# Performance work log

Measured on AMD Instinct MI355X. Metric: run time of the kernel, lower is better.

## Reference

```python
import jax, jax.numpy as jnp
import numpy as np

B, S = 4096, 256
D = 32  # output_size // 4


def setup_inputs() -> dict:
    key = jax.random.key(0)
    ks = jax.random.split(key, 32)
    # continuous features
    cont_p = jax.random.normal(ks[0], (B, S, 3), dtype=jnp.float32)
    cont_c = jax.random.normal(ks[1], (B, S, 2), dtype=jnp.float32)
    # categorical features, per-column vocab sizes from Embedding tables
    vocabs_p = [2, 2, 2, 11, 34]
    cat_p = jnp.stack([
        jax.random.randint(ks[2 + i], (B, S), 0, v, dtype=jnp.int32)
        for i, v in enumerate(vocabs_p)], axis=2)
    vocabs_c = [19, 31]
    cat_c = jnp.stack([
        jax.random.randint(ks[7 + i], (B, S), 0, v, dtype=jnp.int32)
        for i, v in enumerate(vocabs_c)], axis=2)
    lengths = jax.random.randint(ks[9], (B,), 1, S + 1, dtype=jnp.int32)

    def lin(k, fan_in, fan_out):
        bound = 1.0 / np.sqrt(fan_in)
        kw, kb = jax.random.split(k)
        w = jax.random.uniform(kw, (fan_in, fan_out), jnp.float32, -bound, bound)
        b = jax.random.uniform(kb, (fan_out,), jnp.float32, -bound, bound)
        return w, b

    w_p1, b_p1 = lin(ks[10], 3, D)
    w_p2, b_p2 = lin(ks[11], D, D)
    w_c1, b_c1 = lin(ks[12], 2, D)
    w_c2, b_c2 = lin(ks[13], D, D)
    emb_gender = jax.random.normal(ks[14], (2, D), dtype=jnp.float32)
    emb_korean = jax.random.normal(ks[15], (2, D), dtype=jnp.float32)
    emb_primary = jax.random.normal(ks[16], (2, D), dtype=jnp.float32)
    emb_job = jax.random.normal(ks[17], (11, D), dtype=jnp.float32)
    emb_rep = jax.random.normal(ks[18], (34, D), dtype=jnp.float32)
    emb_place = jax.random.normal(ks[19], (19, D), dtype=jnp.float32)
    emb_add = jax.random.normal(ks[20], (31, D), dtype=jnp.float32)
    w_fc1, b_fc1 = lin(ks[21], 128, 64)
    w_fc2, b_fc2 = lin(ks[22], 64, 2)

    return dict(cont_p=cont_p, cont_c=cont_c, cat_p=cat_p, cat_c=cat_c,
                lengths=lengths,
                w_p1=w_p1, b_p1=b_p1, w_p2=w_p2, b_p2=b_p2,
                w_c1=w_c1, b_c1=b_c1, w_c2=w_c2, b_c2=b_c2,
                emb_gender=emb_gender, emb_korean=emb_korean,
                emb_primary=emb_primary, emb_job=emb_job, emb_rep=emb_rep,
                emb_place=emb_place, emb_add=emb_add,
                w_fc1=w_fc1, b_fc1=b_fc1, w_fc2=w_fc2, b_fc2=b_fc2)


def reference(cont_p, cont_c, cat_p, cat_c, lengths,
              w_p1, b_p1, w_p2, b_p2, w_c1, b_c1, w_c2, b_c2,
              emb_gender, emb_korean, emb_primary, emb_job, emb_rep,
              emb_place, emb_add, w_fc1, b_fc1, w_fc2, b_fc2):
    # small per-token MLPs on continuous features -> [B,S,D]
    hp = jax.nn.relu(cont_p @ w_p1 + b_p1) @ w_p2 + b_p2
    hc = jax.nn.relu(cont_c @ w_c1 + b_c1) @ w_c2 + b_c2
    # multi-table embedding lookups, averaged per group -> [B,S,D]
    ep = (emb_gender[cat_p[:, :, 0]] + emb_korean[cat_p[:, :, 1]] +
          emb_primary[cat_p[:, :, 2]] + emb_job[cat_p[:, :, 3]] +
          emb_rep[cat_p[:, :, 4]]) / 5.0
    ec = (emb_place[cat_c[:, :, 0]] + emb_add[cat_c[:, :, 1]]) / 2.0
    # concat order matches torch: (cat_p, cat_c, cont_p, cont_c) -> [B,S,128]
    x = jnp.concatenate([ep, ec, hp, hc], axis=2)
    # ragged mean pool over first lengths[i] positions (masked segment mean)
    mask = (jnp.arange(x.shape[1])[None, :] < lengths[:, None])
    pooled = jnp.sum(x * mask[:, :, None], axis=1) / lengths[:, None].astype(x.dtype)
    # head: relu(fc1) -> relu(fc2); dropout p=0.0 is identity
    h = jax.nn.relu(pooled @ w_fc1 + b_fc1)
    return jax.nn.relu(h @ w_fc2 + b_fc2)
```

## Files before the change

kernel.cpp:

```cpp
#include <hip/hip_runtime.h>


#define BDIM 256

__global__ __launch_bounds__(BDIM, 8)
void mlpreg_kernel(const float* __restrict__ cont_p,
                   const float* __restrict__ cont_c,
                   const int* __restrict__ cat_p,
                   const int* __restrict__ cat_c,
                   const int* __restrict__ lengths,
                   const float* __restrict__ w_p1, const float* __restrict__ b_p1,
                   const float* __restrict__ w_p2, const float* __restrict__ b_p2,
                   const float* __restrict__ w_c1, const float* __restrict__ b_c1,
                   const float* __restrict__ w_c2, const float* __restrict__ b_c2,
                   const float* __restrict__ emb_g,  const float* __restrict__ emb_k,
                   const float* __restrict__ emb_pr, const float* __restrict__ emb_j,
                   const float* __restrict__ emb_r,  const float* __restrict__ emb_pl,
                   const float* __restrict__ emb_a,
                   const float* __restrict__ w_fc1, const float* __restrict__ b_fc1,
                   const float* __restrict__ w_fc2, const float* __restrict__ b_fc2,
                   float* __restrict__ out)
{
    constexpr int S = 256;
    __shared__ float sContP[S * 3];
    __shared__ float sContC[S * 2];
    __shared__ int   hist[96];
    __shared__ int   sBin[4][3];
    __shared__ float sRedP[128], sRedC[128];
    __shared__ float sPacc[64];
    __shared__ float sPooled[128];
    __shared__ float sRedF[BDIM];

    const int tid = threadIdx.x;
    const int b   = blockIdx.x;
    int L = lengths[b];
    if (L < 1) L = 1;
    if (L > S) L = S;
    const float invL = 1.0f / (float)L;
    const float Lf   = (float)L;

    const int*   kp = cat_p  + (size_t)b * (S * 5);
    const int*   kc = cat_c  + (size_t)b * (S * 2);
    const float* gp = cont_p + (size_t)b * (S * 3);
    const float* gc = cont_c + (size_t)b * (S * 2);

    const int n3 = 3 * L, n2 = 2 * L, n5 = 5 * L;
    float rp0 = (tid       < n3) ? gp[tid]       : 0.f;
    float rp1 = (tid + 256 < n3) ? gp[tid + 256] : 0.f;
    float rp2 = (tid + 512 < n3) ? gp[tid + 512] : 0.f;
    float rc0 = (tid       < n2) ? gc[tid]       : 0.f;
    float rc1 = (tid + 256 < n2) ? gc[tid + 256] : 0.f;
    int rk[5];
    #pragma unroll
    for (int j = 0; j < 5; ++j) {
        int ii = tid + 256 * j;
        rk[j] = (ii < n5) ? kp[ii] : -1;
    }
    int rq0 = (tid       < n2) ? kc[tid]       : -1;
    int rq1 = (tid + 256 < n2) ? kc[tid + 256] : -1;

    if (tid < 96) hist[tid] = 0;
    __syncthreads();

    if (tid       < n3) sContP[tid]       = rp0;
    if (tid + 256 < n3) sContP[tid + 256] = rp1;
    if (tid + 512 < n3) sContP[tid + 512] = rp2;
    if (tid       < n2) sContC[tid]       = rc0;
    if (tid + 256 < n2) sContC[tid + 256] = rc1;

    int sg = 0, sk = 0, spr = 0;
    #pragma unroll
    for (int j = 0; j < 5; ++j) {
        int ii = tid + 256 * j;
        if (ii < n5) {
            int col = ii % 5, v = rk[j];
            if      (col == 0) sg  += v;
            else if (col == 1) sk  += v;
            else if (col == 2) spr += v;
            else if (col == 3) atomicAdd(&hist[v], 1);
            else               atomicAdd(&hist[11 + v], 1);
        }
    }
    if (rq0 >= 0) atomicAdd(&hist[((tid & 1) ? 64 : 45) + rq0], 1);
    if (rq1 >= 0) atomicAdd(&hist[((tid & 1) ? 64 : 45) + rq1], 1);

    #pragma unroll
    for (int d = 32; d; d >>= 1) {
        sg  += __shfl_xor(sg,  d);
        sk  += __shfl_xor(sk,  d);
        spr += __shfl_xor(spr, d);
    }
    const int wv = tid >> 6, lane = tid & 63;
    if (lane == 0) { sBin[wv][0] = sg; sBin[wv][1] = sk; sBin[wv][2] = spr; }
    __syncthreads();

    const int g8 = tid >> 5, ch = tid & 31, h = lane >> 5;
    const float wp0 = w_p1[ch], wp1 = w_p1[32 + ch], wp2 = w_p1[64 + ch], bp = b_p1[ch];
    const float wc0 = w_c1[ch], wc1 = w_c1[32 + ch], bc = b_c1[ch];
    float accP = 0.f, accC = 0.f;
    #pragma unroll 2
    for (int t = g8; t < L; t += 8) {
        float c0 = sContP[3 * t], c1 = sContP[3 * t + 1], c2 = sContP[3 * t + 2];
        float d0 = sContC[2 * t], d1 = sContC[2 * t + 1];
        accP += fmaxf(fmaf(c0, wp0, fmaf(c1, wp1, fmaf(c2, wp2, bp))), 0.f);
        accC += fmaxf(fmaf(d0, wc0, fmaf(d1, wc1, bc)), 0.f);
    }
    accP += __shfl_down(accP, 32);
    accC += __shfl_down(accC, 32);
    if (lane < 32) { sRedP[wv * 32 + ch] = accP; sRedC[wv * 32 + ch] = accC; }
    __syncthreads();

    if (wv == 0) {
        float sgT  = (float)(sBin[0][0] + sBin[1][0] + sBin[2][0] + sBin[3][0]);
        float skT  = (float)(sBin[0][1] + sBin[1][1] + sBin[2][1] + sBin[3][1]);
        float sprT = (float)(sBin[0][2] + sBin[1][2] + sBin[2][2] + sBin[3][2]);
        float s = 0.f;
        if (h == 0) {
            s  = fmaf(Lf - sgT,  emb_g[ch],  sgT  * emb_g[32 + ch]);
            s += fmaf(Lf - sprT, emb_pr[ch], sprT * emb_pr[32 + ch]);
            #pragma unroll
            for (int r = 0; r < 6; ++r)  s = fmaf((float)hist[r],      emb_j[r * 32 + ch], s);
            #pragma unroll
            for (int r = 0; r < 17; ++r) s = fmaf((float)hist[11 + r], emb_r[r * 32 + ch], s);
        } else {
            s = fmaf(Lf - skT, emb_k[ch], skT * emb_k[32 + ch]);
            #pragma unroll
            for (int r = 6; r < 11; ++r)  s = fmaf((float)hist[r],      emb_j[r * 32 + ch], s);
            #pragma unroll
            for (int r = 17; r < 34; ++r) s = fmaf((float)hist[11 + r], emb_r[r * 32 + ch], s);
        }
        s += __shfl_down(s, 32);
        if (h == 0) sPooled[ch] = s * (invL * 0.2f);
    } else if (wv == 1) {
        float s = 0.f;
        if (h == 0) {
            #pragma unroll
            for (int r = 0; r < 10; ++r) s = fmaf((float)hist[45 + r], emb_pl[r * 32 + ch], s);
            #pragma unroll
            for (int r = 0; r < 16; ++r) s = fmaf((float)hist[64 + r], emb_a[r * 32 + ch], s);
        } else {
            #pragma unroll
            for (int r = 10; r < 19; ++r) s = fmaf((float)hist[45 + r], emb_pl[r * 32 + ch], s);
            #pragma unroll
            for (int r = 16; r < 31; ++r) s = fmaf((float)hist[64 + r], emb_a[r * 32 + ch], s);
        }
        s += __shfl_down(s, 32);
        if (h == 0) sPooled[32 + ch] = s * (invL * 0.5f);
    } else if (wv == 2) {
        if (lane < 32)
            sPacc[ch] = (sRedP[ch] + sRedP[32 + ch] + sRedP[64 + ch] + sRedP[96 + ch]) * invL;
    } else {
        if (lane < 32)
            sPacc[32 + ch] = (sRedC[ch] + sRedC[32 + ch] + sRedC[64 + ch] + sRedC[96 + ch]) * invL;
    }
    __syncthreads();

    if (wv == 2) {
        const int kb = h * 16;
        float v = (h == 0) ? b_p2[ch] : 0.f;
        #pragma unroll
        for (int k = 0; k < 16; ++k) v = fmaf(sPacc[kb + k], w_p2[(kb + k) * 32 + ch], v);
        v += __shfl_down(v, 32);
        if (h == 0) sPooled[64 + ch] = v;
    } else if (wv == 3) {
        const int kb = h * 16;
        float v = (h == 0) ? b_c2[ch] : 0.f;
        #pragma unroll
        for (int k = 0; k < 16; ++k) v = fmaf(sPacc[32 + kb + k], w_c2[(kb + k) * 32 + ch], v);
        v += __shfl_down(v, 32);
        if (h == 0) sPooled[96 + ch] = v;
    }
    __syncthreads();

    {
        const int o = tid & 63, part = tid >> 6;
        const float* wk = w_fc1 + (size_t)(part * 32) * 64 + o;
        const float* xk = sPooled + part * 32;
        float v0 = 0.f, v1 = 0.f, v2 = 0.f, v3 = 0.f;
        #pragma unroll
        for (int k = 0; k < 32; k += 4) {
            v0 = fmaf(xk[k + 0], wk[(size_t)(k + 0) * 64], v0);
            v1 = fmaf(xk[k + 1], wk[(size_t)(k + 1) * 64], v1);
            v2 = fmaf(xk[k + 2], wk[(size_t)(k + 2) * 64], v2);
            v3 = fmaf(xk[k + 3], wk[(size_t)(k + 3) * 64], v3);
        }
        sRedF[tid] = (v0 + v1) + (v2 + v3);
    }
    __syncthreads();

    if (wv == 0) {
        float hv = b_fc1[lane] + (sRedF[lane] + sRedF[64 + lane])
                               + (sRedF[128 + lane] + sRedF[192 + lane]);
        hv = fmaxf(hv, 0.f);
        float p0 = hv * w_fc2[lane * 2 + 0];
        float p1 = hv * w_fc2[lane * 2 + 1];
        #pragma unroll
        for (int d = 32; d; d >>= 1) {
            p0 += __shfl_xor(p0, d);
            p1 += __shfl_xor(p1, d);
        }
        if (lane == 0) {
            float2 o2;
            o2.x = fmaxf(p0 + b_fc2[0], 0.f);
            o2.y = fmaxf(p1 + b_fc2[1], 0.f);
            *(float2*)&out[(size_t)b * 2] = o2;
        }
    }
}

extern "C" void kernel_launch(void* const* d_in, const int* in_sizes, int n_in,
                              void* d_out, int out_size, void* d_ws, size_t ws_size,
                              hipStream_t stream) {
    const float* cont_p = (const float*)d_in[0];
    const float* cont_c = (const float*)d_in[1];
    const int*   cat_p  = (const int*)d_in[2];
    const int*   cat_c  = (const int*)d_in[3];
    const int*   lens   = (const int*)d_in[4];
    const float* w_p1   = (const float*)d_in[5];
    const float* b_p1   = (const float*)d_in[6];
    const float* w_p2   = (const float*)d_in[7];
    const float* b_p2   = (const float*)d_in[8];
    const float* w_c1   = (const float*)d_in[9];
    const float* b_c1   = (const float*)d_in[10];
    const float* w_c2   = (const float*)d_in[11];
    const float* b_c2   = (const float*)d_in[12];
    const float* emb_g  = (const float*)d_in[13];
    const float* emb_k  = (const float*)d_in[14];
    const float* emb_pr = (const float*)d_in[15];
    const float* emb_j  = (const float*)d_in[16];
    const float* emb_r  = (const float*)d_in[17];
    const float* emb_pl = (const float*)d_in[18];
    const float* emb_a  = (const float*)d_in[19];
    const float* w_fc1  = (const float*)d_in[20];
    const float* b_fc1  = (const float*)d_in[21];
    const float* w_fc2  = (const float*)d_in[22];
    const float* b_fc2  = (const float*)d_in[23];
    float* out = (float*)d_out;

    const int B = 4096;
    hipLaunchKernelGGL(mlpreg_kernel, dim3(B), dim3(BDIM), 0, stream,
                       cont_p, cont_c, cat_p, cat_c, lens,
                       w_p1, b_p1, w_p2, b_p2, w_c1, b_c1, w_c2, b_c2,
                       emb_g, emb_k, emb_pr, emb_j, emb_r, emb_pl, emb_a,
                       w_fc1, b_fc1, w_fc2, b_fc2, out);
}
```

Before: 148.8 us.

## Process four rows per block with register prefetch and split histograms

Each block now handles four batch rows in sequence. While the current row is being computed, the next row's inputs are loaded into registers, so global-load latency overlaps with compute. The shared histogram is duplicated per wave pair to reduce atomic contention, and the final fc1 layer is batched across the four rows so each weight load is reused four times. In exchange the grid shrinks to a quarter of the blocks and the min-blocks launch bound is dropped, which lowers the number of resident waves available to hide latency.

New measurement: 152.6 us. 2.6% more time.

```diff
diff --git a/kernel.cpp b/kernel.cpp
--- a/kernel.cpp
+++ b/kernel.cpp
@@ -2,8 +2,34 @@
 
 
 #define BDIM 256
-
-__global__ __launch_bounds__(BDIM, 8)
+#define RPB 4
+
+struct RowRegs {
+    float p0, p1, p2, c0, c1;
+    int   k0, k1, k2, k3, k4, q0, q1;
+};
+
+__device__ __forceinline__ RowRegs load_row(const float* gp, const float* gc,
+                                            const int* kp, const int* kc,
+                                            int tid, int L) {
+    RowRegs r;
+    const int n3 = 3 * L, n2 = 2 * L, n5 = 5 * L;
+    r.p0 = (tid       < n3) ? gp[tid]       : 0.f;
+    r.p1 = (tid + 256 < n3) ? gp[tid + 256] : 0.f;
+    r.p2 = (tid + 512 < n3) ? gp[tid + 512] : 0.f;
+    r.c0 = (tid       < n2) ? gc[tid]       : 0.f;
+    r.c1 = (tid + 256 < n2) ? gc[tid + 256] : 0.f;
+    r.k0 = (tid        < n5) ? kp[tid]        : -1;
+    r.k1 = (tid + 256  < n5) ? kp[tid + 256]  : -1;
+    r.k2 = (tid + 512  < n5) ? kp[tid + 512]  : -1;
+    r.k3 = (tid + 768  < n5) ? kp[tid + 768]  : -1;
+    r.k4 = (tid + 1024 < n5) ? kp[tid + 1024] : -1;
+    r.q0 = (tid       < n2) ? kc[tid]       : -1;
+    r.q1 = (tid + 256 < n2) ? kc[tid + 256] : -1;
+    return r;
+}
+
+__global__ __launch_bounds__(BDIM)
 void mlpreg_kernel(const float* __restrict__ cont_p,
                    const float* __restrict__ cont_c,
                    const int* __restrict__ cat_p,
@@ -24,186 +50,187 @@
     constexpr int S = 256;
     __shared__ float sContP[S * 3];
     __shared__ float sContC[S * 2];
-    __shared__ int   hist[96];
+    __shared__ int   hist[2][96];
     __shared__ int   sBin[4][3];
     __shared__ float sRedP[128], sRedC[128];
     __shared__ float sPacc[64];
-    __shared__ float sPooled[128];
-    __shared__ float sRedF[BDIM];
-
-    const int tid = threadIdx.x;
-    const int b   = blockIdx.x;
-    int L = lengths[b];
-    if (L < 1) L = 1;
-    if (L > S) L = S;
-    const float invL = 1.0f / (float)L;
-    const float Lf   = (float)L;
-
-    const int*   kp = cat_p  + (size_t)b * (S * 5);
-    const int*   kc = cat_c  + (size_t)b * (S * 2);
-    const float* gp = cont_p + (size_t)b * (S * 3);
-    const float* gc = cont_c + (size_t)b * (S * 2);
-
-    const int n3 = 3 * L, n2 = 2 * L, n5 = 5 * L;
-    float rp0 = (tid       < n3) ? gp[tid]       : 0.f;
-    float rp1 = (tid + 256 < n3) ? gp[tid + 256] : 0.f;
-    float rp2 = (tid + 512 < n3) ? gp[tid + 512] : 0.f;
-    float rc0 = (tid       < n2) ? gc[tid]       : 0.f;
-    float rc1 = (tid + 256 < n2) ? gc[tid + 256] : 0.f;
-    int rk[5];
+    __shared__ float sPooled[RPB][128];
+    __shared__ float sF[4][RPB][64];
+
+    const int tid  = threadIdx.x;
+    const int wv   = tid >> 6, lane = tid & 63;
+    const int ch   = tid & 31, h = lane >> 5, g8 = tid >> 5;
+    const int base = blockIdx.x * RPB;
+
+    int Ls[RPB];
     #pragma unroll
-    for (int j = 0; j < 5; ++j) {
-        int ii = tid + 256 * j;
-        rk[j] = (ii < n5) ? kp[ii] : -1;
-    }
-    int rq0 = (tid       < n2) ? kc[tid]       : -1;
-    int rq1 = (tid + 256 < n2) ? kc[tid + 256] : -1;
-
-    if (tid < 96) hist[tid] = 0;
-    __syncthreads();
-
-    if (tid       < n3) sContP[tid]       = rp0;
-    if (tid + 256 < n3) sContP[tid + 256] = rp1;
-    if (tid + 512 < n3) sContP[tid + 512] = rp2;
-    if (tid       < n2) sContC[tid]       = rc0;
-    if (tid + 256 < n2) sContC[tid + 256] = rc1;
-
-    int sg = 0, sk = 0, spr = 0;
+    for (int r = 0; r < RPB; ++r) {
+        int L = lengths[base + r];
+        Ls[r] = (L < 1) ? 1 : (L > S ? S : L);
+    }
+    const float* gpA[RPB]; const float* gcA[RPB];
+    const int*   kpA[RPB]; const int*   kcA[RPB];
     #pragma unroll
-    for (int j = 0; j < 5; ++j) {
-        int ii = tid + 256 * j;
-        if (ii < n5) {
-            int col = ii % 5, v = rk[j];
-            if      (col == 0) sg  += v;
-            else if (col == 1) sk  += v;
-            else if (col == 2) spr += v;
-            else if (col == 3) atomicAdd(&hist[v], 1);
-            else               atomicAdd(&hist[11 + v], 1);
-        }
-    }
-    if (rq0 >= 0) atomicAdd(&hist[((tid & 1) ? 64 : 45) + rq0], 1);
-    if (rq1 >= 0) atomicAdd(&hist[((tid & 1) ? 64 : 45) + rq1], 1);
-
-    #pragma unroll
-    for (int d = 32; d; d >>= 1) {
-        sg  += __shfl_xor(sg,  d);
-        sk  += __shfl_xor(sk,  d);
-        spr += __shfl_xor(spr, d);
-    }
-    const int wv = tid >> 6, lane = tid & 63;
-    if (lane == 0) { sBin[wv][0] = sg; sBin[wv][1] = sk; sBin[wv][2] = spr; }
-    __syncthreads();
-
-    const int g8 = tid >> 5, ch = tid & 31, h = lane >> 5;
+    for (int r = 0; r < RPB; ++r) {
+        gpA[r] = cont_p + (size_t)(base + r) * (S * 3);
+        gcA[r] = cont_c + (size_t)(base + r) * (S * 2);
+        kpA[r] = cat_p  + (size_t)(base + r) * (S * 5);
+        kcA[r] = cat_c  + (size_t)(base + r) * (S * 2);
+    }
     const float wp0 = w_p1[ch], wp1 = w_p1[32 + ch], wp2 = w_p1[64 + ch], bp = b_p1[ch];
     const float wc0 = w_c1[ch], wc1 = w_c1[32 + ch], bc = b_c1[ch];
-    float accP = 0.f, accC = 0.f;
-    #pragma unroll 2
-    for (int t = g8; t < L; t += 8) {
-        float c0 = sContP[3 * t], c1 = sContP[3 * t + 1], c2 = sContP[3 * t + 2];
-        float d0 = sContC[2 * t], d1 = sContC[2 * t + 1];
-        accP += fmaxf(fmaf(c0, wp0, fmaf(c1, wp1, fmaf(c2, wp2, bp))), 0.f);
-        accC += fmaxf(fmaf(d0, wc0, fmaf(d1, wc1, bc)), 0.f);
-    }
-    accP += __shfl_down(accP, 32);
-    accC += __shfl_down(accC, 32);
-    if (lane < 32) { sRedP[wv * 32 + ch] = accP; sRedC[wv * 32 + ch] = accC; }
+
+    for (int i = tid; i < 192; i += BDIM) ((int*)hist)[i] = 0;
+
+    RowRegs cur = load_row(gpA[0], gcA[0], kpA[0], kcA[0], tid, Ls[0]);
     __syncthreads();
 
-    if (wv == 0) {
-        float sgT  = (float)(sBin[0][0] + sBin[1][0] + sBin[2][0] + sBin[3][0]);
-        float skT  = (float)(sBin[0][1] + sBin[1][1] + sBin[2][1] + sBin[3][1]);
-        float sprT = (float)(sBin[0][2] + sBin[1][2] + sBin[2][2] + sBin[3][2]);
-        float s = 0.f;
-        if (h == 0) {
-            s  = fmaf(Lf - sgT,  emb_g[ch],  sgT  * emb_g[32 + ch]);
-            s += fmaf(Lf - sprT, emb_pr[ch], sprT * emb_pr[32 + ch]);
-            #pragma unroll
-            for (int r = 0; r < 6; ++r)  s = fmaf((float)hist[r],      emb_j[r * 32 + ch], s);
-            #pragma unroll
-            for (int r = 0; r < 17; ++r) s = fmaf((float)hist[11 + r], emb_r[r * 32 + ch], s);
-        } else {
-            s = fmaf(Lf - skT, emb_k[ch], skT * emb_k[32 + ch]);
-            #pragma unroll
-            for (int r = 6; r < 11; ++r)  s = fmaf((float)hist[r],      emb_j[r * 32 + ch], s);
-            #pragma unroll
-            for (int r = 17; r < 34; ++r) s = fmaf((float)hist[11 + r], emb_r[r * 32 + ch], s);
-        }
-        s += __shfl_down(s, 32);
-        if (h == 0) sPooled[ch] = s * (invL * 0.2f);
-    } else if (wv == 1) {
-        float s = 0.f;
-        if (h == 0) {
-            #pragma unroll
-            for (int r = 0; r < 10; ++r) s = fmaf((float)hist[45 + r], emb_pl[r * 32 + ch], s);
-            #pragma unroll
-            for (int r = 0; r < 16; ++r) s = fmaf((float)hist[64 + r], emb_a[r * 32 + ch], s);
-        } else {
-            #pragma unroll
-            for (int r = 10; r < 19; ++r) s = fmaf((float)hist[45 + r], emb_pl[r * 32 + ch], s);
-            #pragma unroll
-            for (int r = 16; r < 31; ++r) s = fmaf((float)hist[64 + r], emb_a[r * 32 + ch], s);
-        }
-        s += __shfl_down(s, 32);
-        if (h == 0) sPooled[32 + ch] = s * (invL * 0.5f);
-    } else if (wv == 2) {
-        if (lane < 32)
-            sPacc[ch] = (sRedP[ch] + sRedP[32 + ch] + sRedP[64 + ch] + sRedP[96 + ch]) * invL;
-    } else {
-        if (lane < 32)
-            sPacc[32 + ch] = (sRedC[ch] + sRedC[32 + ch] + sRedC[64 + ch] + sRedC[96 + ch]) * invL;
-    }
-    __syncthreads();
-
-    if (wv == 2) {
-        const int kb = h * 16;
-        float v = (h == 0) ? b_p2[ch] : 0.f;
-        #pragma unroll
-        for (int k = 0; k < 16; ++k) v = fmaf(sPacc[kb + k], w_p2[(kb + k) * 32 + ch], v);
-        v += __shfl_down(v, 32);
-        if (h == 0) sPooled[64 + ch] = v;
-    } else if (wv == 3) {
-        const int kb = h * 16;
-        float v = (h == 0) ? b_c2[ch] : 0.f;
-        #pragma unroll
-        for (int k = 0; k < 16; ++k) v = fmaf(sPacc[32 + kb + k], w_c2[(kb + k) * 32 + ch], v);
-        v += __shfl_down(v, 32);
-        if (h == 0) sPooled[96 + ch] = v;
-    }
-    __syncthreads();
-
-    {
-        const int o = tid & 63, part = tid >> 6;
-        const float* wk = w_fc1 + (size_t)(part * 32) * 64 + o;
-        const float* xk = sPooled + part * 32;
-        float v0 = 0.f, v1 = 0.f, v2 = 0.f, v3 = 0.f;
-        #pragma unroll
-        for (int k = 0; k < 32; k += 4) {
-            v0 = fmaf(xk[k + 0], wk[(size_t)(k + 0) * 64], v0);
-            v1 = fmaf(xk[k + 1], wk[(size_t)(k + 1) * 64], v1);
-            v2 = fmaf(xk[k + 2], wk[(size_t)(k + 2) * 64], v2);
-            v3 = fmaf(xk[k + 3], wk[(size_t)(k + 3) * 64], v3);
-        }
-        sRedF[tid] = (v0 + v1) + (v2 + v3);
-    }
-    __syncthreads();
-
-    if (wv == 0) {
-        float hv = b_fc1[lane] + (sRedF[lane] + sRedF[64 + lane])
-                               + (sRedF[128 + lane] + sRedF[192 + lane]);
-        hv = fmaxf(hv, 0.f);
-        float p0 = hv * w_fc2[lane * 2 + 0];
-        float p1 = hv * w_fc2[lane * 2 + 1];
+    #pragma unroll
+    for (int r = 0; r < RPB; ++r) {
+        const int   L    = Ls[r];
+        const float Lf   = (float)L;
+        const float invL = 1.0f / Lf;
+
+        sContP[tid]       = cur.p0;
+        sContP[tid + 256] = cur.p1;
+        sContP[tid + 512] = cur.p2;
+        sContC[tid]       = cur.c0;
+        sContC[tid + 256] = cur.c1;
+
+        int sg = 0, sk = 0, spr = 0;
+        int* hc = hist[wv >> 1];
+        {
+            int c0 = tid % 5;
+            int c1 = (c0 + 1) % 5, c2 = (c0 + 2) % 5, c3 = (c0 + 3) % 5, c4 = (c0 + 4) % 5;
+            int v;
+            v = cur.k0; if (v >= 0) { if (c0 == 0) sg += v; else if (c0 == 1) sk += v; else if (c0 == 2) spr += v; else if (c0 == 3) atomicAdd(&hc[v], 1); else atomicAdd(&hc[11 + v], 1); }
+            v = cur.k1; if (v >= 0) { if (c1 == 0) sg += v; else if (c1 == 1) sk += v; else if (c1 == 2) spr += v; else if (c1 == 3) atomicAdd(&hc[v], 1); else atomicAdd(&hc[11 + v], 1); }
+            v = cur.k2; if (v >= 0) { if (c2 == 0) sg += v; else if (c2 == 1) sk += v; else if (c2 == 2) spr += v; else if (c2 == 3) atomicAdd(&hc[v], 1); else atomicAdd(&hc[11 + v], 1); }
+            v = cur.k3; if (v >= 0) { if (c3 == 0) sg += v; else if (c3 == 1) sk += v; else if (c3 == 2) spr += v; else if (c3 == 3) atomicAdd(&hc[v], 1); else atomicAdd(&hc[11 + v], 1); }
+            v = cur.k4; if (v >= 0) { if (c4 == 0) sg += v; else if (c4 == 1) sk += v; else if (c4 == 2) spr += v; else if (c4 == 3) atomicAdd(&hc[v], 1); else atomicAdd(&hc[11 + v], 1); }
+        }
+        if (cur.q0 >= 0) atomicAdd(&hc[((tid & 1) ? 64 : 45) + cur.q0], 1);
+        if (cur.q1 >= 0) atomicAdd(&hc[((tid & 1) ? 64 : 45) + cur.q1], 1);
         #pragma unroll
         for (int d = 32; d; d >>= 1) {
-            p0 += __shfl_xor(p0, d);
-            p1 += __shfl_xor(p1, d);
-        }
+            sg += __shfl_xor(sg, d); sk += __shfl_xor(sk, d); spr += __shfl_xor(spr, d);
+        }
+        if (lane == 0) { sBin[wv][0] = sg; sBin[wv][1] = sk; sBin[wv][2] = spr; }
+        __syncthreads();
+
+        RowRegs nxt;
+        if (r + 1 < RPB)
+            nxt = load_row(gpA[r + 1], gcA[r + 1], kpA[r + 1], kcA[r + 1], tid, Ls[r + 1]);
+
+        float accP = 0.f, accC = 0.f;
+        #pragma unroll 2
+        for (int t = g8; t < L; t += 8) {
+            float c0 = sContP[3 * t], c1 = sContP[3 * t + 1], c2 = sContP[3 * t + 2];
+            float d0 = sContC[2 * t], d1 = sContC[2 * t + 1];
+            accP += fmaxf(fmaf(c0, wp0, fmaf(c1, wp1, fmaf(c2, wp2, bp))), 0.f);
+            accC += fmaxf(fmaf(d0, wc0, fmaf(d1, wc1, bc)), 0.f);
+        }
+        accP += __shfl_down(accP, 32);
+        accC += __shfl_down(accC, 32);
+        if (lane < 32) { sRedP[wv * 32 + ch] = accP; sRedC[wv * 32 + ch] = accC; }
+        __syncthreads();
+
+        if (wv == 0) {
+            float sgT  = (float)(sBin[0][0] + sBin[1][0] + sBin[2][0] + sBin[3][0]);
+            float skT  = (float)(sBin[0][1] + sBin[1][1] + sBin[2][1] + sBin[3][1]);
+            float sprT = (float)(sBin[0][2] + sBin[1][2] + sBin[2][2] + sBin[3][2]);
+            float s = 0.f;
+            if (h == 0) {
+                s  = fmaf(Lf - sgT,  emb_g[ch],  sgT  * emb_g[32 + ch]);
+                s += fmaf(Lf - sprT, emb_pr[ch], sprT * emb_pr[32 + ch]);
+                #pragma unroll
+                for (int q = 0; q < 6; ++q)  s = fmaf((float)(hist[0][q] + hist[1][q]),           emb_j[q * 32 + ch], s);
+                #pragma unroll
+                for (int q = 0; q < 17; ++q) s = fmaf((float)(hist[0][11 + q] + hist[1][11 + q]), emb_r[q * 32 + ch], s);
+            } else {
+                s = fmaf(Lf - skT, emb_k[ch], skT * emb_k[32 + ch]);
+                #pragma unroll
+                for (int q = 6; q < 11; ++q)  s = fmaf((float)(hist[0][q] + hist[1][q]),           emb_j[q * 32 + ch], s);
+                #pragma unroll
+                for (int q = 17; q < 34; ++q) s = fmaf((float)(hist[0][11 + q] + hist[1][11 + q]), emb_r[q * 32 + ch], s);
+            }
+            s += __shfl_down(s, 32);
+            if (h == 0) sPooled[r][ch] = s * (invL * 0.2f);
+            if (lane < 45) { hist[0][lane] = 0; hist[1][lane] = 0; }
+        } else if (wv == 1) {
+            float s = 0.f;
+            if (h == 0) {
+                #pragma unroll
+                for (int q = 0; q < 10; ++q) s = fmaf((float)(hist[0][45 + q] + hist[1][45 + q]), emb_pl[q * 32 + ch], s);
+                #pragma unroll
+                for (int q = 0; q < 16; ++q) s = fmaf((float)(hist[0][64 + q] + hist[1][64 + q]), emb_a[q * 32 + ch], s);
+            } else {
+                #pragma unroll
+                for (int q = 10; q < 19; ++q) s = fmaf((float)(hist[0][45 + q] + hist[1][45 + q]), emb_pl[q * 32 + ch], s);
+                #pragma unroll
+                for (int q = 16; q < 31; ++q) s = fmaf((float)(hist[0][64 + q] + hist[1][64 + q]), emb_a[q * 32 + ch], s);
+            }
+            s += __shfl_down(s, 32);
+            if (h == 0) sPooled[r][32 + ch] = s * (invL * 0.5f);
+            if (lane < 51) { hist[0][45 + lane] = 0; hist[1][45 + lane] = 0; }
+        } else if (wv == 2) {
+            if (lane < 32)
+                sPacc[ch] = (sRedP[ch] + sRedP[32 + ch] + sRedP[64 + ch] + sRedP[96 + ch]) * invL;
+        } else {
+            if (lane < 32)
+                sPacc[32 + ch] = (sRedC[ch] + sRedC[32 + ch] + sRedC[64 + ch] + sRedC[96 + ch]) * invL;
+        }
+        __syncthreads();
+
+        if (wv == 2) {
+            const int kb = h * 16;
+            float v = (h == 0) ? b_p2[ch] : 0.f;
+            #pragma unroll
+            for (int k = 0; k < 16; ++k) v = fmaf(sPacc[kb + k], w_p2[(kb + k) * 32 + ch], v);
+            v += __shfl_down(v, 32);
+            if (h == 0) sPooled[r][64 + ch] = v;
+        } else if (wv == 3) {
+            const int kb = h * 16;
+            float v = (h == 0) ? b_c2[ch] : 0.f;
+            #pragma unroll
+            for (int k = 0; k < 16; ++k) v = fmaf(sPacc[32 + kb + k], w_c2[(kb + k) * 32 + ch], v);
+            v += __shfl_down(v, 32);
+            if (h == 0) sPooled[r][96 + ch] = v;
+        }
+        if (r + 1 < RPB) cur = nxt;
+    }
+    __syncthreads();
+
+    {
+        const int o = tid & 63, q = tid >> 6;
+        const float* wk = w_fc1 + (size_t)(q * 32) * 64 + o;
+        float a0 = 0.f, a1 = 0.f, a2 = 0.f, a3 = 0.f;
+        #pragma unroll
+        for (int k = 0; k < 32; ++k) {
+            float w = wk[(size_t)k * 64];
+            a0 = fmaf(sPooled[0][q * 32 + k], w, a0);
+            a1 = fmaf(sPooled[1][q * 32 + k], w, a1);
+            a2 = fmaf(sPooled[2][q * 32 + k], w, a2);
+            a3 = fmaf(sPooled[3][q * 32 + k], w, a3);
+        }
+        sF[q][0][o] = a0; sF[q][1][o] = a1; sF[q][2][o] = a2; sF[q][3][o] = a3;
+    }
+    __syncthreads();
+
+    {
+        const int o = lane;
+        float hv = b_fc1[o] + (sF[0][wv][o] + sF[1][wv][o])
+                            + (sF[2][wv][o] + sF[3][wv][o]);
+        hv = fmaxf(hv, 0.f);
+        float p0 = hv * w_fc2[o * 2 + 0];
+        float p1 = hv * w_fc2[o * 2 + 1];
+        #pragma unroll
+        for (int d = 32; d; d >>= 1) { p0 += __shfl_xor(p0, d); p1 += __shfl_xor(p1, d); }
         if (lane == 0) {
             float2 o2;
             o2.x = fmaxf(p0 + b_fc2[0], 0.f);
             o2.y = fmaxf(p1 + b_fc2[1], 0.f);
-            *(float2*)&out[(size_t)b * 2] = o2;
+            *(float2*)&out[(size_t)(base + wv) * 2] = o2;
         }
     }
 }
@@ -238,7 +265,7 @@
     float* out = (float*)d_out;
 
     const int B = 4096;
-    hipLaunchKernelGGL(mlpreg_kernel, dim3(B), dim3(BDIM), 0, stream,
+    hipLaunchKernelGGL(mlpreg_kernel, dim3(B / RPB), dim3(BDIM), 0, stream,
                        cont_p, cont_c, cat_p, cat_c, lens,
                        w_p1, b_p1, w_p2, b_p2, w_c1, b_c1, w_c2, b_c2,
                        emb_g, emb_k, emb_pr, emb_j, emb_r, emb_pl, emb_a,
```
